# Performance work log

Measured on AMD Instinct MI355X. Metric: run time of the kernel, lower is better.

Reference implementation:

```python
import jax, jax.numpy as jnp
import numpy as np


def setup_inputs() -> dict:
    key = jax.random.key(0)
    k1, k2 = jax.random.split(key)
    B, M, N, D = 64, 16, 64, 1024
    src = jax.random.normal(k1, (B, N, D), dtype=jnp.float32)
    tgts = jax.random.normal(k2, (B, M, N, D), dtype=jnp.float32)
    return {"src": src, "tgts": tgts}


def reference(src, tgts):
    # loss = sum_{b,m,n} | dot(src[b,n], tgts[b,m,n]) |, returned as shape [1]
    dots = jnp.einsum("bnd,bmnd->bmn", src, tgts)  # [B, M, N]
    loss = jnp.sum(jnp.abs(dots))
    return loss.reshape(1)
```

## Files before the change

kernel.cpp:

```cpp
#include <hip/hip_runtime.h>
#include <stdint.h>


typedef __attribute__((ext_vector_type(4))) float f32x4;
typedef const __attribute__((address_space(1))) void* gvp;
typedef __attribute__((address_space(3))) void* svp;

#define GLDS(gp, lp) \
  __builtin_amdgcn_global_load_lds((gvp)(gp), (svp)(lp), 16, 0, 0)

#define WAITV(n)  asm volatile("s_waitcnt vmcnt(" #n ")" ::: "memory")
#define WAITLGKM() asm volatile("s_waitcnt lgkmcnt(0)" ::: "memory")
#define CFENCE() asm volatile("" ::: "memory")

__global__ __launch_bounds__(256) void orth_loss_main(
    const float* __restrict__ src,
    const float* __restrict__ tgts,
    float* __restrict__ partials)
{
    __shared__ float ring[4][3][1024];
    __shared__ float srcb[4][1024];
    __shared__ float sbuf[4];

    const int wave = threadIdx.x >> 6;
    const int lane = threadIdx.x & 63;

    const int w = blockIdx.x * 4 + wave;
    const int n = w & 63;
    const int b = w >> 6;

    const float* srow = src + ((size_t)(b * 64 + n)) * 1024 + lane * 4;
    const int    base_row = (b * 16) * 64 + n;
    const float* trow = tgts + (size_t)base_row * 1024 + lane * 4;
    const size_t mstride = (size_t)64 * 1024;

#pragma unroll
    for (int k = 0; k < 4; ++k)
        GLDS(srow + k * 256, &srcb[wave][k * 256]);
#pragma unroll
    for (int r = 0; r < 3; ++r) {
#pragma unroll
        for (int k = 0; k < 4; ++k)
            GLDS(trow + r * mstride + k * 256, &ring[wave][r][k * 256]);
    }

    float local = 0.0f;
    f32x4 s0, s1, s2, s3;

#define STEP(MI, DO_ISSUE, WN) do {                                          \
      WAITV(WN);                                                             \
      if ((MI) == 0) {                                                       \
        const f32x4* sb_ = (const f32x4*)&srcb[wave][0];                     \
        s0 = sb_[lane];       s1 = sb_[lane + 64];                           \
        s2 = sb_[lane + 128]; s3 = sb_[lane + 192];                          \
      }                                                                      \
      const f32x4* lb_ = (const f32x4*)&ring[wave][(MI) % 3][0];             \
      const f32x4 t0 = lb_[lane];                                            \
      const f32x4 t1 = lb_[lane + 64];                                       \
      const f32x4 t2 = lb_[lane + 128];                                      \
      const f32x4 t3 = lb_[lane + 192];                                      \
      float dot = 0.0f;                                                      \
      dot = fmaf(t0.x, s0.x, dot); dot = fmaf(t0.y, s0.y, dot);              \
      dot = fmaf(t0.z, s0.z, dot); dot = fmaf(t0.w, s0.w, dot);              \
      dot = fmaf(t1.x, s1.x, dot); dot = fmaf(t1.y, s1.y, dot);              \
      dot = fmaf(t1.z, s1.z, dot); dot = fmaf(t1.w, s1.w, dot);              \
      dot = fmaf(t2.x, s2.x, dot); dot = fmaf(t2.y, s2.y, dot);              \
      dot = fmaf(t2.z, s2.z, dot); dot = fmaf(t2.w, s2.w, dot);              \
      dot = fmaf(t3.x, s3.x, dot); dot = fmaf(t3.y, s3.y, dot);              \
      dot = fmaf(t3.z, s3.z, dot); dot = fmaf(t3.w, s3.w, dot);              \
      CFENCE();                                                              \
      if (DO_ISSUE) {                                                        \
        WAITLGKM();        \
        CFENCE();                                                            \
        _Pragma("unroll")                                                    \
        for (int k = 0; k < 4; ++k)                                          \
            GLDS(trow + ((MI) + 3) * mstride + k * 256,                      \
                 &ring[wave][(MI) % 3][k * 256]);                            \
        CFENCE();                                                            \
      }                                                                      \
      _Pragma("unroll")                                                      \
      for (int off = 32; off > 0; off >>= 1)                                 \
          dot += __shfl_down(dot, off, 64);                                  \
      if (lane == 0) local += fabsf(dot);                                    \
    } while (0)

    STEP( 0, 1, 8);
    STEP( 1, 1, 8);
    STEP( 2, 1, 8);
    STEP( 3, 1, 8);
    STEP( 4, 1, 8);
    STEP( 5, 1, 8);
    STEP( 6, 1, 8);
    STEP( 7, 1, 8);
    STEP( 8, 1, 8);
    STEP( 9, 1, 8);
    STEP(10, 1, 8);
    STEP(11, 1, 8);
    STEP(12, 1, 8);
    STEP(13, 0, 8);
    STEP(14, 0, 4);
    STEP(15, 0, 0);
#undef STEP

    if (lane == 0) sbuf[wave] = local;
    __syncthreads();
    if (threadIdx.x == 0)
        partials[blockIdx.x] = sbuf[0] + sbuf[1] + sbuf[2] + sbuf[3];
}

__global__ __launch_bounds__(256) void reduce_partials(
    const float* __restrict__ partials, float* __restrict__ out, int n)
{
    __shared__ float sb[4];
    const int lane = threadIdx.x & 63;
    const int wv   = threadIdx.x >> 6;
    float s = 0.0f;
    for (int i = threadIdx.x; i < n; i += 256) s += partials[i];
#pragma unroll
    for (int off = 32; off > 0; off >>= 1) s += __shfl_down(s, off, 64);
    if (lane == 0) sb[wv] = s;
    __syncthreads();
    if (threadIdx.x == 0) out[0] = sb[0] + sb[1] + sb[2] + sb[3];
}

extern "C" void kernel_launch(void* const* d_in, const int* in_sizes, int n_in,
                              void* d_out, int out_size, void* d_ws, size_t ws_size,
                              hipStream_t stream) {
    const float* src  = (const float*)d_in[0];
    const float* tgts = (const float*)d_in[1];
    float* out      = (float*)d_out;
    float* partials = (float*)d_ws;

    const int total_waves = in_sizes[0] / 1024;
    const int blocks = total_waves / 4;

    orth_loss_main<<<blocks, 256, 0, stream>>>(src, tgts, partials);
    reduce_partials<<<1, 256, 0, stream>>>(partials, out, blocks);
}
```

Measured before the change: 49.69 us.

## Deepen LDS ring to four stages and defer wave reductions to the end

Raises the tgts prefetch ring from three to four stages per wave, keeps the src row in registers loaded directly from global memory instead of staging it through LDS, and stores per-step partial dots so the 16 cross-lane shuffle reductions run after the streaming loop. This aims to keep more memory requests in flight and to remove shuffle work from between load issues. It costs more registers for the 16 stored partials, and shared memory use stays the same.

```diff
diff --git a/kernel.cpp b/kernel.cpp
--- a/kernel.cpp
+++ b/kernel.cpp
@@ -9,17 +9,16 @@
 #define GLDS(gp, lp) \
   __builtin_amdgcn_global_load_lds((gvp)(gp), (svp)(lp), 16, 0, 0)
 
-#define WAITV(n)  asm volatile("s_waitcnt vmcnt(" #n ")" ::: "memory")
+#define WAITV(n)   asm volatile("s_waitcnt vmcnt(" #n ")" ::: "memory")
 #define WAITLGKM() asm volatile("s_waitcnt lgkmcnt(0)" ::: "memory")
-#define CFENCE() asm volatile("" ::: "memory")
+#define CFENCE()   asm volatile("" ::: "memory")
 
 __global__ __launch_bounds__(256) void orth_loss_main(
     const float* __restrict__ src,
     const float* __restrict__ tgts,
     float* __restrict__ partials)
 {
-    __shared__ float ring[4][3][1024];
-    __shared__ float srcb[4][1024];
+    __shared__ float ring[4][4][1024];
     __shared__ float sbuf[4];
 
     const int wave = threadIdx.x >> 6;
@@ -29,32 +28,30 @@
     const int n = w & 63;
     const int b = w >> 6;
 
-    const float* srow = src + ((size_t)(b * 64 + n)) * 1024 + lane * 4;
+    const f32x4* __restrict__ sp =
+        reinterpret_cast<const f32x4*>(src + ((size_t)(b * 64 + n)) * 1024);
+    const f32x4 s0 = sp[lane];
+    const f32x4 s1 = sp[lane + 64];
+    const f32x4 s2 = sp[lane + 128];
+    const f32x4 s3 = sp[lane + 192];
+
     const int    base_row = (b * 16) * 64 + n;
     const float* trow = tgts + (size_t)base_row * 1024 + lane * 4;
     const size_t mstride = (size_t)64 * 1024;
 
+    CFENCE();
 #pragma unroll
-    for (int k = 0; k < 4; ++k)
-        GLDS(srow + k * 256, &srcb[wave][k * 256]);
-#pragma unroll
-    for (int r = 0; r < 3; ++r) {
+    for (int r = 0; r < 4; ++r) {
 #pragma unroll
         for (int k = 0; k < 4; ++k)
             GLDS(trow + r * mstride + k * 256, &ring[wave][r][k * 256]);
     }
 
-    float local = 0.0f;
-    f32x4 s0, s1, s2, s3;
+    float p[16];
 
 #define STEP(MI, DO_ISSUE, WN) do {                                          \
       WAITV(WN);                                                             \
-      if ((MI) == 0) {                                                       \
-        const f32x4* sb_ = (const f32x4*)&srcb[wave][0];                     \
-        s0 = sb_[lane];       s1 = sb_[lane + 64];                           \
-        s2 = sb_[lane + 128]; s3 = sb_[lane + 192];                          \
-      }                                                                      \
-      const f32x4* lb_ = (const f32x4*)&ring[wave][(MI) % 3][0];             \
+      const f32x4* lb_ = (const f32x4*)&ring[wave][(MI) % 4][0];             \
       const f32x4 t0 = lb_[lane];                                            \
       const f32x4 t1 = lb_[lane + 64];                                       \
       const f32x4 t2 = lb_[lane + 128];                                      \
@@ -68,39 +65,46 @@
       dot = fmaf(t2.z, s2.z, dot); dot = fmaf(t2.w, s2.w, dot);              \
       dot = fmaf(t3.x, s3.x, dot); dot = fmaf(t3.y, s3.y, dot);              \
       dot = fmaf(t3.z, s3.z, dot); dot = fmaf(t3.w, s3.w, dot);              \
+      p[MI] = dot;                                                           \
       CFENCE();                                                              \
       if (DO_ISSUE) {                                                        \
-        WAITLGKM();        \
+        WAITLGKM();           \
         CFENCE();                                                            \
         _Pragma("unroll")                                                    \
         for (int k = 0; k < 4; ++k)                                          \
-            GLDS(trow + ((MI) + 3) * mstride + k * 256,                      \
-                 &ring[wave][(MI) % 3][k * 256]);                            \
+            GLDS(trow + ((MI) + 4) * mstride + k * 256,                      \
+                 &ring[wave][(MI) % 4][k * 256]);                            \
         CFENCE();                                                            \
       }                                                                      \
-      _Pragma("unroll")                                                      \
-      for (int off = 32; off > 0; off >>= 1)                                 \
-          dot += __shfl_down(dot, off, 64);                                  \
-      if (lane == 0) local += fabsf(dot);                                    \
     } while (0)
 
-    STEP( 0, 1, 8);
-    STEP( 1, 1, 8);
-    STEP( 2, 1, 8);
-    STEP( 3, 1, 8);
-    STEP( 4, 1, 8);
-    STEP( 5, 1, 8);
-    STEP( 6, 1, 8);
-    STEP( 7, 1, 8);
-    STEP( 8, 1, 8);
-    STEP( 9, 1, 8);
-    STEP(10, 1, 8);
-    STEP(11, 1, 8);
-    STEP(12, 1, 8);
+    STEP( 0, 1, 12);
+    STEP( 1, 1, 12);
+    STEP( 2, 1, 12);
+    STEP( 3, 1, 12);
+    STEP( 4, 1, 12);
+    STEP( 5, 1, 12);
+    STEP( 6, 1, 12);
+    STEP( 7, 1, 12);
+    STEP( 8, 1, 12);
+    STEP( 9, 1, 12);
+    STEP(10, 1, 12);
+    STEP(11, 1, 12);
+    STEP(12, 0, 12);
     STEP(13, 0, 8);
     STEP(14, 0, 4);
     STEP(15, 0, 0);
 #undef STEP
+
+    float local = 0.0f;
+#pragma unroll
+    for (int mi = 0; mi < 16; ++mi) {
+        float d = p[mi];
+#pragma unroll
+        for (int off = 32; off > 0; off >>= 1)
+            d += __shfl_down(d, off, 64);
+        if (lane == 0) local += fabsf(d);
+    }
 
     if (lane == 0) sbuf[wave] = local;
     __syncthreads();
```

Result: no change. 50.47 us (+1.6%).
